# Kernel optimization log

Hardware: AMD Instinct MI355X
Metric: run time of the kernel (lower is better)

The kernel has to match this reference:

```python
import jax, jax.numpy as jnp
import numpy as np

B, N, V, J, K = 2, 16384, 10475, 55, 6
WEIGHT_STD2 = 2.0 * 0.1 ** 2  # 0.02


def setup_inputs() -> dict:
    ks = jax.random.split(jax.random.key(0), 5)
    x = jax.random.normal(ks[0], (B, N, 3), dtype=jnp.float32)
    # cam = [scale, tx, ty]; scale kept positive/near 1
    scale = jax.random.uniform(ks[1], (B, 1), minval=0.8, maxval=1.2)
    trans = jax.random.normal(ks[1], (B, 2)) * 0.05
    cam = jnp.concatenate([scale, trans], axis=-1).astype(jnp.float32)
    # skinning weights: sparse-ish simplex rows
    lbs_weights = jax.nn.softmax(4.0 * jax.random.normal(ks[2], (V, J)), axis=-1).astype(jnp.float32)
    # per-vertex rigid-ish transforms: identity + noise
    verts_transform = (jnp.eye(4, dtype=jnp.float32)[None, None]
                       + 0.1 * jax.random.normal(ks[3], (B, V, 4, 4), dtype=jnp.float32))
    posed_verts = jax.random.normal(ks[4], (B, V, 3), dtype=jnp.float32)
    return {"x": x, "cam": cam, "lbs_weights": lbs_weights,
            "verts_transform": verts_transform, "posed_verts": posed_verts}


def _orth_proj_inv(x, cam):
    # inverse of batch_orth_proj: undo scale, undo xy translation
    scale = cam[:, 0].reshape(-1, 1, 1)
    t = cam[:, 1:3].reshape(-1, 1, 2)
    xy = x[..., :2] / scale - t
    z = x[..., 2:] / scale
    return jnp.concatenate([xy, z], axis=-1)


def _knn(points, verts, k):
    # brute-force KNN on squared euclidean distance (matches knn_points)
    p2 = jnp.sum(points * points, axis=-1, keepdims=True)          # [B,N,1]
    v2 = jnp.sum(verts * verts, axis=-1)                           # [B,V]
    cross = jnp.einsum('bnd,bvd->bnv', points, verts)              # [B,N,V]
    d2 = p2 + v2[:, None, :] - 2.0 * cross
    neg_d, idx = jax.lax.top_k(-d2, k)                             # smallest k
    return jnp.maximum(-neg_d, 0.0), idx


def reference(x, cam, lbs_weights, verts_transform, posed_verts):
    posed_x = _orth_proj_inv(x, cam)                               # [B,N,3]

    # KNN is under torch.no_grad in the original
    dists, idx = _knn(jax.lax.stop_gradient(posed_x),
                      jax.lax.stop_gradient(posed_verts), K)       # [B,N,K]

    # gather skinning weights of neighbors: lbs_weights shared across batch
    w_nb = lbs_weights[idx]                                        # [B,N,K,J]
    conf = jnp.exp(-jnp.sum(jnp.abs(w_nb - w_nb[..., 0:1, :]), axis=-1) / WEIGHT_STD2)
    conf = (conf > 0.9).astype(posed_x.dtype)                      # [B,N,K]

    w = jnp.exp(-dists) * conf
    w = w / jnp.sum(w, axis=-1, keepdims=True)                     # [B,N,K]

    # batched gather of per-vertex transforms
    T_nb = jax.vmap(lambda T, i: T[i])(verts_transform, idx)       # [B,N,K,4,4]
    x_transform = jnp.einsum('bnk,bnkij->bnij', w, T_nb)           # [B,N,4,4]

    # batch_transform: apply rigid transform to posed points
    cano_x = (jnp.einsum('bnij,bnj->bni', x_transform[..., :3, :3], posed_x)
              + x_transform[..., :3, 3])                           # [B,N,3]
    return cano_x
```

## Files before the change

### kernel.cpp

```cpp
#include <hip/hip_runtime.h>
#include <math.h>

#define B_ 2
#define N_ 16384
#define V_ 10475
#define J_ 55
#define K_ 6

constexpr int   NB      = 512;
constexpr int   PB      = 2 * NB;
constexpr int   SSTRIDE = 16384;
constexpr float ZLO     = -6.0f;
constexpr float ZHI     =  6.0f;
constexpr float HBIN    = (ZHI - ZLO) / (float)NB;
constexpr float INVH    = (float)NB / (ZHI - ZLO);
constexpr float R2OUT   = 5.76f;

__device__ __forceinline__ int zbin(float z) {
    int b = (int)floorf((z - ZLO) * INVH);
    return min(max(b, 0), NB - 1);
}

__device__ __forceinline__ double shfl_d(double v, int src) {
    int lo = __double2loint(v), hi = __double2hiint(v);
    lo = __shfl(lo, src, 64);
    hi = __shfl(hi, src, 64);
    return __hiloint2double(hi, lo);
}

__device__ __forceinline__ void async16(void* lds, const void* g) {
    __builtin_amdgcn_global_load_lds(
        (const __attribute__((address_space(1))) void*)g,
        (__attribute__((address_space(3))) void*)lds, 16, 0, 0);
}

__global__ __launch_bounds__(1024) void build_kernel(const float* __restrict__ pverts,
                                                     const float* __restrict__ x,
                                                     const float* __restrict__ cam,
                                                     float4* __restrict__ pvs,
                                                     int* __restrict__ vidx,
                                                     int* __restrict__ psort,
                                                     int* __restrict__ binStartV) {
    __shared__ int hist[PB];
    __shared__ int cur[PB];
    const int t = threadIdx.x;
    const int b = blockIdx.x >> 1;
    const bool vertsKind = (blockIdx.x & 1) == 0;

    if (t < PB) hist[t] = 0;
    __syncthreads();

    const float cs = cam[b * 3 + 0], ctx = cam[b * 3 + 1], cty = cam[b * 3 + 2];

    if (vertsKind) {
        for (int i = t; i < V_; i += 1024)
            atomicAdd(&hist[zbin(pverts[((size_t)(b * V_ + i)) * 3 + 2])], 1);
    } else {
        for (int i = t; i < N_; i += 1024) {
            size_t g = (size_t)(b * N_ + i) * 3;
            float px = x[g] / cs - ctx, py = x[g + 1] / cs - cty, pz = x[g + 2] / cs;
            float r2 = px * px + py * py + pz * pz;
            atomicAdd(&hist[zbin(pz) + ((r2 > R2OUT) ? NB : 0)], 1);
        }
    }
    __syncthreads();

    for (int off = 1; off < PB; off <<= 1) {
        int v = 0;
        if (t < PB && t >= off) v = hist[t - off];
        __syncthreads();
        if (t < PB) hist[t] += v;
        __syncthreads();
    }
    if (t < PB) {
        int ex = (t == 0) ? 0 : hist[t - 1];
        cur[t] = ex;
        if (vertsKind && t < NB) binStartV[b * (NB + 1) + t] = ex;
    }
    if (vertsKind && t == 0) binStartV[b * (NB + 1) + NB] = hist[NB - 1];
    __syncthreads();

    if (vertsKind) {
        for (int i = t; i < V_; i += 1024) {
            size_t g = (size_t)(b * V_ + i) * 3;
            float vx = pverts[g], vy = pverts[g + 1], vz = pverts[g + 2];
            int pos = atomicAdd(&cur[zbin(vz)], 1);
            pvs[b * SSTRIDE + pos] = make_float4(vx, vy, vz, vx * vx + vy * vy + vz * vz);
            vidx[b * SSTRIDE + pos] = i;
        }
    } else {
        for (int i = t; i < N_; i += 1024) {
            size_t g = (size_t)(b * N_ + i) * 3;
            float px = x[g] / cs - ctx, py = x[g + 1] / cs - cty, pz = x[g + 2] / cs;
            float r2 = px * px + py * py + pz * pz;
            int pos = atomicAdd(&cur[zbin(pz) + ((r2 > R2OUT) ? NB : 0)], 1);
            psort[b * N_ + pos] = b * N_ + i;
        }
    }
}

__global__ __launch_bounds__(1024, 8) void knn_kernel(const float4* __restrict__ pvs,
                                                      const int* __restrict__ vidx,
                                                      const int* __restrict__ binStartV,
                                                      const int* __restrict__ psort,
                                                      const float* __restrict__ x,
                                                      const float* __restrict__ cam,
                                                      const float* __restrict__ lbs,
                                                      const float* __restrict__ vt,
                                                      float* __restrict__ out) {
    __shared__ float4 tile[2048];
    __shared__ unsigned int cK[16][67][6];
    __shared__ float sMax[16];

    const int tid = threadIdx.x, lane = tid & 63, wid = tid >> 6;
    const int b   = blockIdx.x >> 8;
    const int blk = blockIdx.x & 255;
    const int pid = psort[b * N_ + blk * 64 + lane];

    const float cs = cam[b * 3 + 0], ctx = cam[b * 3 + 1], cty = cam[b * 3 + 2];
    const float Px = x[pid * 3 + 0] / cs - ctx;
    const float Py = x[pid * 3 + 1] / cs - cty;
    const float Pz = x[pid * 3 + 2] / cs;
    const float Ax = -2.f * Px, Ay = -2.f * Py, Az = -2.f * Pz;
    const float Cc = Px * Px + Py * Py + Pz * Pz + 1.0e-4f;

    float zmin = Pz, zmax = Pz;
#pragma unroll
    for (int m = 1; m <= 32; m <<= 1) {
        zmin = fminf(zmin, __shfl_xor(zmin, m, 64));
        zmax = fmaxf(zmax, __shfl_xor(zmax, m, 64));
    }

    const int* bs = binStartV + b * (NB + 1);
    int cbin = zbin(0.5f * (zmin + zmax));
    int center = (bs[cbin] + bs[cbin + 1]) >> 1;
    int lo = center - 1024;
    lo = max(0, min(lo, V_ - 2048));
    int hi = lo + 2048;

    unsigned int bK[6];
#pragma unroll
    for (int t = 0; t < 6; ++t) bK[t] = 0xFFFFFFFFu;

    const float4* pb = pvs + b * SSTRIDE;

#define SCAN_RANGE(RL, CNT)                                                    \
    for (int i = wid; i < (CNT); i += 16) {                                    \
        float4 q = tile[i];                  \
        float d2 = fmaf(Ax, q.x, fmaf(Ay, q.y, fmaf(Az, q.z, Cc + q.w)));      \
        unsigned int key = (__float_as_uint(d2) & 0xFFFFC000u)                 \
                         | (unsigned int)((RL) + i);                           \
        if (key < bK[5]) {                                                     \
            unsigned int kk = key;                                             \
            _Pragma("unroll")                                                  \
            for (int t = 0; t < 6; ++t) {                                      \
                unsigned int mn = min(kk, bK[t]);                              \
                kk = max(kk, bK[t]);                                           \
                bK[t] = mn;                                                    \
            }                                                                  \
        }                                                                      \
    }

#define PMERGE(E)                                                              \
    {                                                                          \
        const int pj = lane & 15, pp = (wid << 2) + (lane >> 4);               \
        _Pragma("unroll")                                                      \
        for (int t = 0; t < 6; ++t) (E)[t] = cK[pj][pp][t];                    \
        (E)[6] = 0xFFFFFFFFu; (E)[7] = 0xFFFFFFFFu;                            \
        _Pragma("unroll")                                                      \
        for (int s = 1; s <= 8; s <<= 1) {                                     \
            unsigned int Bt[8], Cv[8];                                         \
            _Pragma("unroll")                                                  \
            for (int t = 0; t < 8; ++t)                                        \
                Bt[t] = (unsigned int)__shfl_xor((int)(E)[t], s, 64);          \
            _Pragma("unroll")                                                  \
            for (int t = 0; t < 8; ++t) Cv[t] = min((E)[t], Bt[7 - t]);        \
            CEU(0, 4) CEU(1, 5) CEU(2, 6) CEU(3, 7)                            \
            CEU(0, 2) CEU(1, 3) CEU(4, 6) CEU(5, 7)                            \
            CEU(0, 1) CEU(2, 3) CEU(4, 5) CEU(6, 7)                            \
            _Pragma("unroll")                                                  \
            for (int t = 0; t < 8; ++t) (E)[t] = Cv[t];                        \
        }                                                                      \
    }
#define CEU(a, c) { unsigned int mn_ = min(Cv[a], Cv[c]); Cv[c] = max(Cv[a], Cv[c]); Cv[a] = mn_; }

    async16(&tile[tid], &pb[lo + tid]);
    async16(&tile[tid + 1024], &pb[lo + 1024 + tid]);
    __syncthreads();
    SCAN_RANGE(lo, 2048)

#pragma unroll
    for (int t = 0; t < 6; ++t) cK[wid][lane][t] = bK[t];
    __syncthreads();
    {
        unsigned int E1[8];
        PMERGE(E1)
        float g = __uint_as_float(E1[5] | 0x3FFFu);
#pragma unroll
        for (int m = 1; m <= 32; m <<= 1)
            g = fmaxf(g, __shfl_xor(g, m, 64));
        if (lane == 0) sMax[wid] = g;
    }
    __syncthreads();
    float G = sMax[0];
#pragma unroll
    for (int t = 1; t < 16; ++t) G = fmaxf(G, sMax[t]);

    while (true) {
        float bl = 3.0e38f, br = 3.0e38f;
        if (lo > 0) {
            int j = zbin(pb[lo - 1].z);
            bl = (j >= NB - 1) ? 0.f
               : fmaxf(0.f, zmin - (ZLO + (float)(j + 1) * HBIN));
        }
        if (hi < V_) {
            int j = zbin(pb[hi].z);
            br = (j <= 0) ? 0.f
               : fmaxf(0.f, (ZLO + (float)j * HBIN) - zmax);
        }
        bool canL = (lo > 0)  && (bl * bl < G);
        bool canR = (hi < V_) && (br * br < G);
        if (!canL && !canR) break;
        bool left = canL && (!canR || bl <= br);
        int rl, rh;
        if (left) { rh = lo; rl = max(0, lo - 1024); lo = rl; }
        else      { rl = hi; rh = min(V_, hi + 1024); hi = rh; }
        __syncthreads();
        int cnt = rh - rl;
        int cntPad = (cnt + 63) & ~63;
        if (tid < cntPad) async16(&tile[tid], &pb[rl + tid]);
        __syncthreads();
        SCAN_RANGE(rl, cnt)
    }
#undef SCAN_RANGE

    __syncthreads();
#pragma unroll
    for (int t = 0; t < 6; ++t) cK[wid][lane][t] = bK[t];
    __syncthreads();
    unsigned int E[8];
    PMERGE(E)
#undef PMERGE
#undef CEU

    const int lj = lane & 15;
    const int gb = lane & ~15;
    const int pl = (wid << 2) + (lane >> 4);
    const int pid2 = psort[b * N_ + blk * 64 + pl];

    const float Qx = x[pid2 * 3 + 0] / cs - ctx;
    const float Qy = x[pid2 * 3 + 1] / cs - cty;
    const float Qz = x[pid2 * 3 + 2] / cs;

    double myd = 1.0e300;
    int mygi = 0x7FFFFFFF;
    if (lj < 8) {
        unsigned int key = E[lj];
        if (key != 0xFFFFFFFFu) {
            int pos = (int)(key & 0x3FFFu);
            mygi = vidx[b * SSTRIDE + pos];
            float4 vq = pb[pos];
            const double csd = (double)cs;
            const double PX = (double)x[pid2 * 3 + 0] / csd - (double)ctx;
            const double PY = (double)x[pid2 * 3 + 1] / csd - (double)cty;
            const double PZ = (double)x[pid2 * 3 + 2] / csd;
            double vx = (double)vq.x, vy = (double)vq.y, vz = (double)vq.z;
            double v2 = vx * vx + vy * vy + vz * vz;
            double P2 = PX * PX + PY * PY + PZ * PZ;
            double dot = PX * vx + PY * vy + PZ * vz;
            myd = P2 + v2 - 2.0 * dot;
        }
    }
    double dd[8];
    int ii[8];
#pragma unroll
    for (int t = 0; t < 8; ++t) { dd[t] = shfl_d(myd, gb + t); ii[t] = __shfl(mygi, gb + t, 64); }
#define CE_(a, c) { \
        bool sw_ = (dd[a] > dd[c]) || (dd[a] == dd[c] && ii[a] > ii[c]); \
        double dt_ = sw_ ? dd[a] : dd[c]; dd[a] = sw_ ? dd[c] : dd[a]; dd[c] = dt_; \
        int it_ = sw_ ? ii[a] : ii[c]; ii[a] = sw_ ? ii[c] : ii[a]; ii[c] = it_; }
#pragma unroll
    for (int r = 0; r < 4; ++r) {
        CE_(0, 1) CE_(2, 3) CE_(4, 5) CE_(6, 7)
        CE_(1, 2) CE_(3, 4) CE_(5, 6)
    }
#undef CE_

    const int i0 = (ii[0] < V_) ? ii[0] : 0;
    float r0v[4];
#pragma unroll
    for (int r = 0; r < 4; ++r) {
        int e = lj + (r << 4);
        r0v[r] = (e < J_) ? lbs[i0 * J_ + e] : 0.f;
    }
    float wgt[K_];
    wgt[0] = expf(-fmaxf((float)dd[0], 0.f));
#pragma unroll
    for (int k = 1; k < K_; ++k) {
        int gk = (ii[k] < V_) ? ii[k] : 0;
        float sv = 0.f;
#pragma unroll
        for (int r = 0; r < 4; ++r) {
            int e = lj + (r << 4);
            sv += (e < J_) ? fabsf(lbs[gk * J_ + e] - r0v[r]) : 0.f;
        }
#pragma unroll
        for (int m = 1; m <= 8; m <<= 1) sv += __shfl_xor(sv, m, 64);
        wgt[k] = (sv < 0.0021072103f) ? expf(-fmaxf((float)dd[k], 0.f)) : 0.f;
    }
    float wsum = ((wgt[0] + wgt[1]) + (wgt[2] + wgt[3])) + (wgt[4] + wgt[5]);
    float inv = 1.f / wsum;

    float acc = 0.f;
#pragma unroll
    for (int k = 0; k < K_; ++k) {
        int gk = (ii[k] < V_) ? ii[k] : 0;
        acc += (wgt[k] * inv) * vt[((size_t)(b * V_ + gk)) * 16 + lj];
    }
    const int c = lj & 3;
    float pc = (c == 0) ? Qx : (c == 1) ? Qy : (c == 2) ? Qz : 1.f;
    float part = acc * pc;
    part += __shfl_xor(part, 1, 64);
    part += __shfl_xor(part, 2, 64);
    if (lj == 0)      out[pid2 * 3 + 0] = part;
    else if (lj == 4) out[pid2 * 3 + 1] = part;
    else if (lj == 8) out[pid2 * 3 + 2] = part;
}

extern "C" void kernel_launch(void* const* d_in, const int* in_sizes, int n_in,
                              void* d_out, int out_size, void* d_ws, size_t ws_size,
                              hipStream_t stream) {
    const float* x      = (const float*)d_in[0];
    const float* cam    = (const float*)d_in[1];
    const float* lbs    = (const float*)d_in[2];
    const float* vt     = (const float*)d_in[3];
    const float* pverts = (const float*)d_in[4];
    float* out = (float*)d_out;

    char* ws = (char*)d_ws;
    int* binStartV = (int*)ws;
    float4* pvs = (float4*)(ws + 4112);
    int* vidx  = (int*)((char*)pvs + (size_t)B_ * SSTRIDE * 16);
    int* psort = vidx + B_ * SSTRIDE;

    build_kernel<<<4, 1024, 0, stream>>>(pverts, x, cam, pvs, vidx, psort, binStartV);
    knn_kernel<<<B_ * (N_ / 64), 1024, 0, stream>>>(pvs, vidx, binStartV, psort,
                                                    x, cam, lbs, vt, out);
}
```

Measured before the change: 215.7 us.

## Split wide-radius query blocks into four vertex-range workers with last-block merge

Query blocks whose points lie outside the inner radius (sorted to the end by the build pass) are now brute-forced over the whole vertex set, split into four quarter-range blocks. Each block writes its partial top-8 keys to global memory, and the last block to finish, tracked with an atomic counter, merges them and runs the skinning epilogue. This is meant to fix load imbalance, where a few blocks with far-away points expanded their z-window over most vertices serially. The cost is extra global traffic for partial keys, an atomic plus threadfence handshake, and a grid of 2048 blocks in which many of the extra blocks exit immediately.

Measured after the change: 549.8 us. 155% more time.

```diff
diff --git a/kernel.cpp b/kernel.cpp
--- a/kernel.cpp
+++ b/kernel.cpp
@@ -40,7 +40,9 @@
                                                      float4* __restrict__ pvs,
                                                      int* __restrict__ vidx,
                                                      int* __restrict__ psort,
-                                                     int* __restrict__ binStartV) {
+                                                     int* __restrict__ binStartV,
+                                                     int* __restrict__ pcut,
+                                                     int* __restrict__ wcnt) {
     __shared__ int hist[PB];
     __shared__ int cur[PB];
     const int t = threadIdx.x;
@@ -48,6 +50,7 @@
     const bool vertsKind = (blockIdx.x & 1) == 0;
 
     if (t < PB) hist[t] = 0;
+    if (!vertsKind && t < 256) wcnt[b * 256 + t] = 0;
     __syncthreads();
 
     const float cs = cam[b * 3 + 0], ctx = cam[b * 3 + 1], cty = cam[b * 3 + 2];
@@ -78,6 +81,7 @@
         if (vertsKind && t < NB) binStartV[b * (NB + 1) + t] = ex;
     }
     if (vertsKind && t == 0) binStartV[b * (NB + 1) + NB] = hist[NB - 1];
+    if (!vertsKind && t == NB - 1) pcut[b] = hist[t];
     __syncthreads();
 
     if (vertsKind) {
@@ -97,6 +101,100 @@
             psort[b * N_ + pos] = b * N_ + i;
         }
     }
+}
+
+__device__ __forceinline__ void epilogue_fn(const unsigned int* E,
+                                            int lane, int wid,
+                                            float cs, float ctx, float cty,
+                                            const float4* pb,
+                                            const int* __restrict__ vidxb,
+                                            const int* __restrict__ psortb,
+                                            const float* __restrict__ x,
+                                            const float* __restrict__ lbs,
+                                            const float* __restrict__ vt,
+                                            float* __restrict__ out, int bV) {
+    const int lj = lane & 15;
+    const int gb = lane & ~15;
+    const int pl = (wid << 2) + (lane >> 4);
+    const int pid2 = psortb[pl];
+
+    const float Qx = x[pid2 * 3 + 0] / cs - ctx;
+    const float Qy = x[pid2 * 3 + 1] / cs - cty;
+    const float Qz = x[pid2 * 3 + 2] / cs;
+
+    double myd = 1.0e300;
+    int mygi = 0x7FFFFFFF;
+    if (lj < 8) {
+        unsigned int key = E[lj];
+        if (key != 0xFFFFFFFFu) {
+            int pos = (int)(key & 0x3FFFu);
+            mygi = vidxb[pos];
+            float4 vq = pb[pos];
+            const double csd = (double)cs;
+            const double PX = (double)x[pid2 * 3 + 0] / csd - (double)ctx;
+            const double PY = (double)x[pid2 * 3 + 1] / csd - (double)cty;
+            const double PZ = (double)x[pid2 * 3 + 2] / csd;
+            double vx = (double)vq.x, vy = (double)vq.y, vz = (double)vq.z;
+            double v2 = vx * vx + vy * vy + vz * vz;
+            double P2 = PX * PX + PY * PY + PZ * PZ;
+            double dot = PX * vx + PY * vy + PZ * vz;
+            myd = P2 + v2 - 2.0 * dot;
+        }
+    }
+    double dd[8];
+    int ii[8];
+#pragma unroll
+    for (int t = 0; t < 8; ++t) { dd[t] = shfl_d(myd, gb + t); ii[t] = __shfl(mygi, gb + t, 64); }
+#define CE_(a, c) { \
+        bool sw_ = (dd[a] > dd[c]) || (dd[a] == dd[c] && ii[a] > ii[c]); \
+        double dt_ = sw_ ? dd[a] : dd[c]; dd[a] = sw_ ? dd[c] : dd[a]; dd[c] = dt_; \
+        int it_ = sw_ ? ii[a] : ii[c]; ii[a] = sw_ ? ii[c] : ii[a]; ii[c] = it_; }
+#pragma unroll
+    for (int r = 0; r < 4; ++r) {
+        CE_(0, 1) CE_(2, 3) CE_(4, 5) CE_(6, 7)
+        CE_(1, 2) CE_(3, 4) CE_(5, 6)
+    }
+#undef CE_
+
+    const int i0 = (ii[0] < V_) ? ii[0] : 0;
+    float r0v[4];
+#pragma unroll
+    for (int r = 0; r < 4; ++r) {
+        int e = lj + (r << 4);
+        r0v[r] = (e < J_) ? lbs[i0 * J_ + e] : 0.f;
+    }
+    float wgt[K_];
+    wgt[0] = expf(-fmaxf((float)dd[0], 0.f));
+#pragma unroll
+    for (int k = 1; k < K_; ++k) {
+        int gk = (ii[k] < V_) ? ii[k] : 0;
+        float sv = 0.f;
+#pragma unroll
+        for (int r = 0; r < 4; ++r) {
+            int e = lj + (r << 4);
+            sv += (e < J_) ? fabsf(lbs[gk * J_ + e] - r0v[r]) : 0.f;
+        }
+#pragma unroll
+        for (int m = 1; m <= 8; m <<= 1) sv += __shfl_xor(sv, m, 64);
+        wgt[k] = (sv < 0.0021072103f) ? expf(-fmaxf((float)dd[k], 0.f)) : 0.f;
+    }
+    float wsum = ((wgt[0] + wgt[1]) + (wgt[2] + wgt[3])) + (wgt[4] + wgt[5]);
+    float inv = 1.f / wsum;
+
+    float acc = 0.f;
+#pragma unroll
+    for (int k = 0; k < K_; ++k) {
+        int gk = (ii[k] < V_) ? ii[k] : 0;
+        acc += (wgt[k] * inv) * vt[((size_t)(bV + gk)) * 16 + lj];
+    }
+    const int c = lj & 3;
+    float pc = (c == 0) ? Qx : (c == 1) ? Qy : (c == 2) ? Qz : 1.f;
+    float part = acc * pc;
+    part += __shfl_xor(part, 1, 64);
+    part += __shfl_xor(part, 2, 64);
+    if (lj == 0)      out[pid2 * 3 + 0] = part;
+    else if (lj == 4) out[pid2 * 3 + 1] = part;
+    else if (lj == 8) out[pid2 * 3 + 2] = part;
 }
 
 __global__ __launch_bounds__(1024, 8) void knn_kernel(const float4* __restrict__ pvs,
@@ -107,14 +205,32 @@
                                                       const float* __restrict__ cam,
                                                       const float* __restrict__ lbs,
                                                       const float* __restrict__ vt,
+                                                      const int* __restrict__ pcut,
+                                                      int* __restrict__ wcnt,
+                                                      unsigned int* __restrict__ wkeys,
                                                       float* __restrict__ out) {
     __shared__ float4 tile[2048];
     __shared__ unsigned int cK[16][67][6];
     __shared__ float sMax[16];
+    __shared__ int amLast;
 
     const int tid = threadIdx.x, lane = tid & 63, wid = tid >> 6;
-    const int b   = blockIdx.x >> 8;
-    const int blk = blockIdx.x & 255;
+    const int b = blockIdx.x >> 10;
+    const int r = blockIdx.x & 1023;
+    const int pc = pcut[b];
+    const int wideStart = pc >> 6;
+    int blk, q;
+    bool isWide;
+    if (r < 256) {
+        blk = r; q = 0; isWide = (blk >= wideStart);
+    } else {
+        int j = r - 256;
+        int widx = j / 3;
+        q = 1 + (j % 3);
+        if (widx >= 256 - wideStart) return;
+        blk = wideStart + widx;
+        isWide = true;
+    }
     const int pid = psort[b * N_ + blk * 64 + lane];
 
     const float cs = cam[b * 3 + 0], ctx = cam[b * 3 + 1], cty = cam[b * 3 + 2];
@@ -124,30 +240,18 @@
     const float Ax = -2.f * Px, Ay = -2.f * Py, Az = -2.f * Pz;
     const float Cc = Px * Px + Py * Py + Pz * Pz + 1.0e-4f;
 
-    float zmin = Pz, zmax = Pz;
-#pragma unroll
-    for (int m = 1; m <= 32; m <<= 1) {
-        zmin = fminf(zmin, __shfl_xor(zmin, m, 64));
-        zmax = fmaxf(zmax, __shfl_xor(zmax, m, 64));
-    }
-
-    const int* bs = binStartV + b * (NB + 1);
-    int cbin = zbin(0.5f * (zmin + zmax));
-    int center = (bs[cbin] + bs[cbin + 1]) >> 1;
-    int lo = center - 1024;
-    lo = max(0, min(lo, V_ - 2048));
-    int hi = lo + 2048;
-
     unsigned int bK[6];
 #pragma unroll
     for (int t = 0; t < 6; ++t) bK[t] = 0xFFFFFFFFu;
 
     const float4* pb = pvs + b * SSTRIDE;
+    const int* vidxb = vidx + b * SSTRIDE;
+    const int* psortb = psort + b * N_ + blk * 64;
 
 #define SCAN_RANGE(RL, CNT)                                                    \
     for (int i = wid; i < (CNT); i += 16) {                                    \
-        float4 q = tile[i];                  \
-        float d2 = fmaf(Ax, q.x, fmaf(Ay, q.y, fmaf(Az, q.z, Cc + q.w)));      \
+        float4 qv = tile[i];                 \
+        float d2 = fmaf(Ax, qv.x, fmaf(Ay, qv.y, fmaf(Az, qv.z, Cc + qv.w)));  \
         unsigned int key = (__float_as_uint(d2) & 0xFFFFC000u)                 \
                          | (unsigned int)((RL) + i);                           \
         if (key < bK[5]) {                                                     \
@@ -184,147 +288,127 @@
     }
 #define CEU(a, c) { unsigned int mn_ = min(Cv[a], Cv[c]); Cv[c] = max(Cv[a], Cv[c]); Cv[a] = mn_; }
 
-    async16(&tile[tid], &pb[lo + tid]);
-    async16(&tile[tid + 1024], &pb[lo + 1024 + tid]);
-    __syncthreads();
-    SCAN_RANGE(lo, 2048)
-
-#pragma unroll
-    for (int t = 0; t < 6; ++t) cK[wid][lane][t] = bK[t];
-    __syncthreads();
-    {
-        unsigned int E1[8];
-        PMERGE(E1)
-        float g = __uint_as_float(E1[5] | 0x3FFFu);
-#pragma unroll
-        for (int m = 1; m <= 32; m <<= 1)
-            g = fmaxf(g, __shfl_xor(g, m, 64));
-        if (lane == 0) sMax[wid] = g;
-    }
-    __syncthreads();
-    float G = sMax[0];
-#pragma unroll
-    for (int t = 1; t < 16; ++t) G = fmaxf(G, sMax[t]);
-
-    while (true) {
-        float bl = 3.0e38f, br = 3.0e38f;
-        if (lo > 0) {
-            int j = zbin(pb[lo - 1].z);
-            bl = (j >= NB - 1) ? 0.f
-               : fmaxf(0.f, zmin - (ZLO + (float)(j + 1) * HBIN));
-        }
-        if (hi < V_) {
-            int j = zbin(pb[hi].z);
-            br = (j <= 0) ? 0.f
-               : fmaxf(0.f, (ZLO + (float)j * HBIN) - zmax);
-        }
-        bool canL = (lo > 0)  && (bl * bl < G);
-        bool canR = (hi < V_) && (br * br < G);
-        if (!canL && !canR) break;
-        bool left = canL && (!canR || bl <= br);
-        int rl, rh;
-        if (left) { rh = lo; rl = max(0, lo - 1024); lo = rl; }
-        else      { rl = hi; rh = min(V_, hi + 1024); hi = rh; }
-        __syncthreads();
-        int cnt = rh - rl;
-        int cntPad = (cnt + 63) & ~63;
-        if (tid < cntPad) async16(&tile[tid], &pb[rl + tid]);
-        __syncthreads();
-        SCAN_RANGE(rl, cnt)
+    if (!isWide) {
+        float zmin = Pz, zmax = Pz;
+#pragma unroll
+        for (int m = 1; m <= 32; m <<= 1) {
+            zmin = fminf(zmin, __shfl_xor(zmin, m, 64));
+            zmax = fmaxf(zmax, __shfl_xor(zmax, m, 64));
+        }
+        const int* bs = binStartV + b * (NB + 1);
+        int cbin = zbin(0.5f * (zmin + zmax));
+        int center = (bs[cbin] + bs[cbin + 1]) >> 1;
+        int lo = center - 1024;
+        lo = max(0, min(lo, V_ - 2048));
+        int hi = lo + 2048;
+
+        async16(&tile[tid], &pb[lo + tid]);
+        async16(&tile[tid + 1024], &pb[lo + 1024 + tid]);
+        __syncthreads();
+        SCAN_RANGE(lo, 2048)
+
+#pragma unroll
+        for (int t = 0; t < 6; ++t) cK[wid][lane][t] = bK[t];
+        __syncthreads();
+        {
+            unsigned int E1[8];
+            PMERGE(E1)
+            float g = __uint_as_float(E1[5] | 0x3FFFu);
+#pragma unroll
+            for (int m = 1; m <= 32; m <<= 1)
+                g = fmaxf(g, __shfl_xor(g, m, 64));
+            if (lane == 0) sMax[wid] = g;
+        }
+        __syncthreads();
+        float G = sMax[0];
+#pragma unroll
+        for (int t = 1; t < 16; ++t) G = fmaxf(G, sMax[t]);
+
+        while (true) {
+            float bl = 3.0e38f, br = 3.0e38f;
+            if (lo > 0) {
+                int j = zbin(pb[lo - 1].z);
+                bl = (j >= NB - 1) ? 0.f
+                   : fmaxf(0.f, zmin - (ZLO + (float)(j + 1) * HBIN));
+            }
+            if (hi < V_) {
+                int j = zbin(pb[hi].z);
+                br = (j <= 0) ? 0.f
+                   : fmaxf(0.f, (ZLO + (float)j * HBIN) - zmax);
+            }
+            bool canL = (lo > 0)  && (bl * bl < G);
+            bool canR = (hi < V_) && (br * br < G);
+            if (!canL && !canR) break;
+            bool left = canL && (!canR || bl <= br);
+            int rl, rh;
+            if (left) { rh = lo; rl = max(0, lo - 1024); lo = rl; }
+            else      { rl = hi; rh = min(V_, hi + 1024); hi = rh; }
+            __syncthreads();
+            int cnt = rh - rl;
+            int cntPad = (cnt + 63) & ~63;
+            if (tid < cntPad) async16(&tile[tid], &pb[rl + tid]);
+            __syncthreads();
+            SCAN_RANGE(rl, cnt)
+        }
+
+        __syncthreads();
+#pragma unroll
+        for (int t = 0; t < 6; ++t) cK[wid][lane][t] = bK[t];
+        __syncthreads();
+        unsigned int E[8];
+        PMERGE(E)
+        epilogue_fn(E, lane, wid, cs, ctx, cty, pb, vidxb, psortb,
+                    x, lbs, vt, out, b * V_);
+    } else {
+        const int qlo = (V_ * q) >> 2;
+        const int qhi = (V_ * (q + 1)) >> 2;
+        for (int t0 = qlo; t0 < qhi; t0 += 2048) {
+            int cnt = min(2048, qhi - t0);
+            int cntPad = (cnt + 63) & ~63;
+            __syncthreads();
+            if (tid < cntPad) async16(&tile[tid], &pb[t0 + tid]);
+            if (tid + 1024 < cntPad) async16(&tile[tid + 1024], &pb[t0 + tid + 1024]);
+            __syncthreads();
+            SCAN_RANGE(t0, cnt)
+        }
+#pragma unroll
+        for (int t = 0; t < 6; ++t) cK[wid][lane][t] = bK[t];
+        __syncthreads();
+        unsigned int E[8];
+        PMERGE(E)
+
+        const int lj = lane & 15;
+        const int pl = (wid << 2) + (lane >> 4);
+        const size_t base = ((size_t)(b * 256 + blk) * 64 + pl) * 32;
+        if (lj < 8) wkeys[base + q * 8 + lj] = E[lj];
+        __threadfence();
+        __syncthreads();
+        if (tid == 0) amLast = (atomicAdd(&wcnt[b * 256 + blk], 1) == 3);
+        __syncthreads();
+        if (!amLast) return;
+        __threadfence();
+
+        unsigned int E2[8];
+#pragma unroll
+        for (int t = 0; t < 8; ++t) E2[t] = 0xFFFFFFFFu;
+        volatile const unsigned int* wk = wkeys + base;
+        for (int j = 0; j < 32; ++j) {
+            unsigned int kk = wk[j];
+            if (kk < E2[7]) {
+#pragma unroll
+                for (int u = 0; u < 8; ++u) {
+                    unsigned int mn = min(kk, E2[u]);
+                    kk = max(kk, E2[u]);
+                    E2[u] = mn;
+                }
+            }
+        }
+        epilogue_fn(E2, lane, wid, cs, ctx, cty, pb, vidxb, psortb,
+                    x, lbs, vt, out, b * V_);
     }
 #undef SCAN_RANGE
-
-    __syncthreads();
-#pragma unroll
-    for (int t = 0; t < 6; ++t) cK[wid][lane][t] = bK[t];
-    __syncthreads();
-    unsigned int E[8];
-    PMERGE(E)
 #undef PMERGE
 #undef CEU
-
-    const int lj = lane & 15;
-    const int gb = lane & ~15;
-    const int pl = (wid << 2) + (lane >> 4);
-    const int pid2 = psort[b * N_ + blk * 64 + pl];
-
-    const float Qx = x[pid2 * 3 + 0] / cs - ctx;
-    const float Qy = x[pid2 * 3 + 1] / cs - cty;
-    const float Qz = x[pid2 * 3 + 2] / cs;
-
-    double myd = 1.0e300;
-    int mygi = 0x7FFFFFFF;
-    if (lj < 8) {
-        unsigned int key = E[lj];
-        if (key != 0xFFFFFFFFu) {
-            int pos = (int)(key & 0x3FFFu);
-            mygi = vidx[b * SSTRIDE + pos];
-            float4 vq = pb[pos];
-            const double csd = (double)cs;
-            const double PX = (double)x[pid2 * 3 + 0] / csd - (double)ctx;
-            const double PY = (double)x[pid2 * 3 + 1] / csd - (double)cty;
-            const double PZ = (double)x[pid2 * 3 + 2] / csd;
-            double vx = (double)vq.x, vy = (double)vq.y, vz = (double)vq.z;
-            double v2 = vx * vx + vy * vy + vz * vz;
-            double P2 = PX * PX + PY * PY + PZ * PZ;
-            double dot = PX * vx + PY * vy + PZ * vz;
-            myd = P2 + v2 - 2.0 * dot;
-        }
-    }
-    double dd[8];
-    int ii[8];
-#pragma unroll
-    for (int t = 0; t < 8; ++t) { dd[t] = shfl_d(myd, gb + t); ii[t] = __shfl(mygi, gb + t, 64); }
-#define CE_(a, c) { \
-        bool sw_ = (dd[a] > dd[c]) || (dd[a] == dd[c] && ii[a] > ii[c]); \
-        double dt_ = sw_ ? dd[a] : dd[c]; dd[a] = sw_ ? dd[c] : dd[a]; dd[c] = dt_; \
-        int it_ = sw_ ? ii[a] : ii[c]; ii[a] = sw_ ? ii[c] : ii[a]; ii[c] = it_; }
-#pragma unroll
-    for (int r = 0; r < 4; ++r) {
-        CE_(0, 1) CE_(2, 3) CE_(4, 5) CE_(6, 7)
-        CE_(1, 2) CE_(3, 4) CE_(5, 6)
-    }
-#undef CE_
-
-    const int i0 = (ii[0] < V_) ? ii[0] : 0;
-    float r0v[4];
-#pragma unroll
-    for (int r = 0; r < 4; ++r) {
-        int e = lj + (r << 4);
-        r0v[r] = (e < J_) ? lbs[i0 * J_ + e] : 0.f;
-    }
-    float wgt[K_];
-    wgt[0] = expf(-fmaxf((float)dd[0], 0.f));
-#pragma unroll
-    for (int k = 1; k < K_; ++k) {
-        int gk = (ii[k] < V_) ? ii[k] : 0;
-        float sv = 0.f;
-#pragma unroll
-        for (int r = 0; r < 4; ++r) {
-            int e = lj + (r << 4);
-            sv += (e < J_) ? fabsf(lbs[gk * J_ + e] - r0v[r]) : 0.f;
-        }
-#pragma unroll
-        for (int m = 1; m <= 8; m <<= 1) sv += __shfl_xor(sv, m, 64);
-        wgt[k] = (sv < 0.0021072103f) ? expf(-fmaxf((float)dd[k], 0.f)) : 0.f;
-    }
-    float wsum = ((wgt[0] + wgt[1]) + (wgt[2] + wgt[3])) + (wgt[4] + wgt[5]);
-    float inv = 1.f / wsum;
-
-    float acc = 0.f;
-#pragma unroll
-    for (int k = 0; k < K_; ++k) {
-        int gk = (ii[k] < V_) ? ii[k] : 0;
-        acc += (wgt[k] * inv) * vt[((size_t)(b * V_ + gk)) * 16 + lj];
-    }
-    const int c = lj & 3;
-    float pc = (c == 0) ? Qx : (c == 1) ? Qy : (c == 2) ? Qz : 1.f;
-    float part = acc * pc;
-    part += __shfl_xor(part, 1, 64);
-    part += __shfl_xor(part, 2, 64);
-    if (lj == 0)      out[pid2 * 3 + 0] = part;
-    else if (lj == 4) out[pid2 * 3 + 1] = part;
-    else if (lj == 8) out[pid2 * 3 + 2] = part;
 }
 
 extern "C" void kernel_launch(void* const* d_in, const int* in_sizes, int n_in,
@@ -339,11 +423,18 @@
 
     char* ws = (char*)d_ws;
     int* binStartV = (int*)ws;
-    float4* pvs = (float4*)(ws + 4112);
+    int* pcut      = binStartV + 2 * (NB + 1);
+    int* wcnt      = pcut + 2;
+    char* p16 = (char*)(wcnt + 512);
+    size_t off = (((size_t)(p16 - ws)) + 15) & ~(size_t)15;
+    float4* pvs = (float4*)(ws + off);
     int* vidx  = (int*)((char*)pvs + (size_t)B_ * SSTRIDE * 16);
     int* psort = vidx + B_ * SSTRIDE;
-
-    build_kernel<<<4, 1024, 0, stream>>>(pverts, x, cam, pvs, vidx, psort, binStartV);
-    knn_kernel<<<B_ * (N_ / 64), 1024, 0, stream>>>(pvs, vidx, binStartV, psort,
-                                                    x, cam, lbs, vt, out);
-}
+    unsigned int* wkeys = (unsigned int*)(psort + B_ * N_);
+
+    build_kernel<<<4, 1024, 0, stream>>>(pverts, x, cam, pvs, vidx, psort,
+                                         binStartV, pcut, wcnt);
+    knn_kernel<<<B_ * 1024, 1024, 0, stream>>>(pvs, vidx, binStartV, psort,
+                                               x, cam, lbs, vt, pcut, wcnt,
+                                               wkeys, out);
+}
```
